# Performance work log

Hardware: AMD Instinct MI355X
Metric: run time of the kernel (lower is better)

## Reference

```python
import jax, jax.numpy as jnp
import numpy as np

BN_EPS = 1e-5

def _segment_mean(vals, idx, num_segments):
    s = jax.ops.segment_sum(vals, idx, num_segments=num_segments)
    cnt = jax.ops.segment_sum(jnp.ones((vals.shape[0],), vals.dtype), idx, num_segments=num_segments)
    return s / jnp.maximum(cnt, 1.0)[:, None]


def setup_inputs() -> dict:
    N, E, L = 50000, 800000, 1600000
    ND, ED = 256, 128
    key = jax.random.key(0)
    ks = jax.random.split(key, 8)
    return {
        "x": jax.random.normal(ks[0], (N, ND), jnp.float32),
        "edge_attr": jax.random.normal(ks[1], (E, ED), jnp.float32),
        "W_proj": jax.random.normal(ks[2], (ED, ND), jnp.float32) / np.sqrt(ND),
        "W1": jax.random.normal(ks[3], (ED, ED), jnp.float32) / np.sqrt(ED),
        "b1": jnp.zeros((ED,), jnp.float32),
        "prelu_a": jnp.full((1,), 0.25, jnp.float32),
        "bn_gamma": jnp.ones((ED,), jnp.float32),
        "bn_beta": jnp.zeros((ED,), jnp.float32),
        "edge_index": jax.random.randint(ks[4], (2, E), 0, N, jnp.int32),
        "line_graph_edge_index": jax.random.randint(ks[5], (2, L), 0, E, jnp.int32),
    }


def reference(x, edge_attr, W_proj, W1, b1, prelu_a, bn_gamma, bn_beta, edge_index, line_graph_edge_index):
    N = x.shape[0]
    E = edge_attr.shape[0]
    src, dst = edge_index[0], edge_index[1]
    # project once then gather (same math as gathering then projecting)
    px = x @ W_proj.T  # [N, edge_dim]
    fused = edge_attr + (px[src] + px[dst]) * 0.5  # [E, edge_dim]
    # line-graph message passing: scatter-mean over destination edges
    line_src, line_dst = line_graph_edge_index[0], line_graph_edge_index[1]
    agg = _segment_mean(fused[line_src], line_dst, E)  # [E, edge_dim]
    # edge update: Linear -> PReLU -> BatchNorm1d (training-mode batch stats)
    h = agg @ W1.T + b1
    h = jnp.where(h >= 0, h, prelu_a * h)
    mean = jnp.mean(h, axis=0)
    var = jnp.mean(jnp.square(h - mean), axis=0)  # biased, as torch BN
    h = (h - mean) * jax.lax.rsqrt(var + BN_EPS) * bn_gamma + bn_beta
    fused = fused + h
    # aggregate edges back to nodes (scatter-mean over dst)
    node_updates = _segment_mean(fused, dst, N)  # [N, edge_dim]
    return node_updates
```

## Files before the change

kernel.cpp:

```cpp
#include <hip/hip_runtime.h>
#include <cstdint>

#define BN_EPS 1e-5f

template<int K, bool EPI>
__global__ __launch_bounds__(256) void gemm_kernel(
    const float* __restrict__ A,
    const float* __restrict__ W,
    const float* __restrict__ bias,
    const float* __restrict__ prelu_a,
    float* __restrict__ C,
    float* __restrict__ bnsum,
    float* __restrict__ bnsumsq,
    int M)
{
    constexpr int BM = 64, BN = 128, BK = 32;
    __shared__ float aT[BK][BM + 4];
    __shared__ float wT[BK][BN];
    __shared__ float red_s[BN];
    __shared__ float red_q[BN];

    const int tid = threadIdx.x;
    const int tx = tid & 31;
    const int ty = tid >> 5;
    const int row0 = blockIdx.x * BM;

    float acc[8][4];
#pragma unroll
    for (int r = 0; r < 8; ++r)
#pragma unroll
        for (int c = 0; c < 4; ++c) acc[r][c] = 0.f;

    for (int k0 = 0; k0 < K; k0 += BK) {
#pragma unroll
        for (int rep = 0; rep < 2; ++rep) {
            int r  = (tid >> 3) + rep * 32;
            int kq = tid & 7;
            int grow = row0 + r;
            float4 v = make_float4(0.f, 0.f, 0.f, 0.f);
            if (grow < M)
                v = *(const float4*)(A + (size_t)grow * K + k0 + 4 * kq);
            aT[4*kq+0][r] = v.x;
            aT[4*kq+1][r] = v.y;
            aT[4*kq+2][r] = v.z;
            aT[4*kq+3][r] = v.w;
        }
#pragma unroll
        for (int rep = 0; rep < 4; ++rep) {
            int j  = tid & 127;
            int kh = tid >> 7;
            int kk = kh * 16 + rep * 4;
            float4 v = *(const float4*)(W + (size_t)j * K + k0 + kk);
            wT[kk+0][j] = v.x;
            wT[kk+1][j] = v.y;
            wT[kk+2][j] = v.z;
            wT[kk+3][j] = v.w;
        }
        __syncthreads();
#pragma unroll
        for (int k = 0; k < BK; ++k) {
            float4 w4 = *(const float4*)&wT[k][4*tx];
            float4 a0 = *(const float4*)&aT[k][8*ty];
            float4 a1 = *(const float4*)&aT[k][8*ty+4];
            float av[8] = {a0.x,a0.y,a0.z,a0.w,a1.x,a1.y,a1.z,a1.w};
            float wv[4] = {w4.x,w4.y,w4.z,w4.w};
#pragma unroll
            for (int r = 0; r < 8; ++r)
#pragma unroll
                for (int c = 0; c < 4; ++c)
                    acc[r][c] = fmaf(av[r], wv[c], acc[r][c]);
        }
        __syncthreads();
    }

    if (!EPI) {
#pragma unroll
        for (int r = 0; r < 8; ++r) {
            int grow = row0 + 8*ty + r;
            if (grow < M) {
                float4 o = make_float4(acc[r][0], acc[r][1], acc[r][2], acc[r][3]);
                *(float4*)(C + (size_t)grow * BN + 4*tx) = o;
            }
        }
    } else {
        float b[4];
#pragma unroll
        for (int c = 0; c < 4; ++c) b[c] = bias[4*tx + c];
        float pa = prelu_a[0];
        if (tid < BN) { red_s[tid] = 0.f; red_q[tid] = 0.f; }
        __syncthreads();
        float lsum[4] = {0,0,0,0}, lsq[4] = {0,0,0,0};
#pragma unroll
        for (int r = 0; r < 8; ++r) {
            int grow = row0 + 8*ty + r;
            if (grow < M) {
                float vv[4];
#pragma unroll
                for (int c = 0; c < 4; ++c) {
                    float v = acc[r][c] + b[c];
                    v = (v >= 0.f) ? v : pa * v;
                    vv[c] = v;
                    lsum[c] += v;
                    lsq[c]  += v * v;
                }
                float4 o = make_float4(vv[0], vv[1], vv[2], vv[3]);
                *(float4*)(C + (size_t)grow * BN + 4*tx) = o;
            }
        }
#pragma unroll
        for (int c = 0; c < 4; ++c) {
            atomicAdd(&red_s[4*tx + c], lsum[c]);
            atomicAdd(&red_q[4*tx + c], lsq[c]);
        }
        __syncthreads();
        if (tid < BN) {
            atomicAdd(&bnsum[tid],   red_s[tid]);
            atomicAdd(&bnsumsq[tid], red_q[tid]);
        }
    }
}

__global__ __launch_bounds__(256) void fuse_kernel(
    const float* __restrict__ edge_attr, const float* __restrict__ px,
    const int* __restrict__ src, const int* __restrict__ dst,
    float* __restrict__ fused, int E)
{
    size_t i = (size_t)blockIdx.x * blockDim.x + threadIdx.x;
    size_t total = (size_t)E * 32;
    if (i >= total) return;
    int e = (int)(i >> 5);
    int q = (int)(i & 31);
    int s = src[e], d = dst[e];
    float4 ea = ((const float4*)edge_attr)[i];
    float4 ps = ((const float4*)px)[(size_t)s * 32 + q];
    float4 pd = ((const float4*)px)[(size_t)d * 32 + q];
    float4 o;
    o.x = ea.x + 0.5f * (ps.x + pd.x);
    o.y = ea.y + 0.5f * (ps.y + pd.y);
    o.z = ea.z + 0.5f * (ps.z + pd.z);
    o.w = ea.w + 0.5f * (ps.w + pd.w);
    ((float4*)fused)[i] = o;
}

__global__ __launch_bounds__(256) void hist_kernel(
    const int* __restrict__ idx, int* __restrict__ deg, int n)
{
    int i = blockIdx.x * 256 + threadIdx.x;
    if (i < n) atomicAdd(&deg[idx[i]], 1);
}

__global__ __launch_bounds__(256) void scan_local_kernel(
    const int* __restrict__ deg, int* __restrict__ excl,
    int* __restrict__ bsum, int n)
{
    __shared__ int ts[256];
    int t = threadIdx.x;
    int base = blockIdx.x * 2048 + t * 8;
    int v[8]; int s = 0;
#pragma unroll
    for (int j = 0; j < 8; ++j) { v[j] = (base + j < n) ? deg[base + j] : 0; s += v[j]; }
    ts[t] = s; __syncthreads();
    for (int off = 1; off < 256; off <<= 1) {
        int x = (t >= off) ? ts[t - off] : 0;
        __syncthreads();
        ts[t] += x;
        __syncthreads();
    }
    if (t == 255) bsum[blockIdx.x] = ts[255];
    int run = ts[t] - s;
#pragma unroll
    for (int j = 0; j < 8; ++j) {
        if (base + j < n) excl[base + j] = run;
        run += v[j];
    }
}

__global__ __launch_bounds__(256) void scan_blocks_kernel(int* __restrict__ bsum, int nb)
{
    __shared__ int ts[256];
    __shared__ int carry_s;
    int t = threadIdx.x;
    if (t == 0) carry_s = 0;
    __syncthreads();
    for (int c0 = 0; c0 < nb; c0 += 256) {
        int v = (c0 + t < nb) ? bsum[c0 + t] : 0;
        ts[t] = v; __syncthreads();
        for (int off = 1; off < 256; off <<= 1) {
            int x = (t >= off) ? ts[t - off] : 0;
            __syncthreads();
            ts[t] += x;
            __syncthreads();
        }
        int carry = carry_s;
        if (c0 + t < nb) bsum[c0 + t] = carry + ts[t] - v;
        int tot = ts[255];
        __syncthreads();
        if (t == 0) carry_s = carry + tot;
        __syncthreads();
    }
}

__global__ __launch_bounds__(256) void scan_add_kernel(
    int* __restrict__ rowptr, const int* __restrict__ bsum,
    int* __restrict__ cursor, int n, int total)
{
    int i = blockIdx.x * 256 + threadIdx.x;
    if (i == 0) rowptr[n] = total;
    if (i >= n) return;
    int v = rowptr[i] + bsum[i >> 11];
    rowptr[i] = v;
    cursor[i] = v;
}

__global__ __launch_bounds__(256) void fill_kernel(
    const int* __restrict__ dsti, const int* __restrict__ vals,
    int* __restrict__ cursor, int* __restrict__ adj, int n)
{
    int i = blockIdx.x * 256 + threadIdx.x;
    if (i >= n) return;
    int pos = atomicAdd(&cursor[dsti[i]], 1);
    adj[pos] = vals ? vals[i] : i;
}

__global__ __launch_bounds__(256) void gather_line_kernel(
    const float* __restrict__ fused, const int* __restrict__ rowptr,
    const int* __restrict__ adj, float* __restrict__ agg, int E)
{
    int w = (int)(((size_t)blockIdx.x * 256 + threadIdx.x) >> 6);
    int lane = threadIdx.x & 63;
    if (w >= E) return;
    int s0 = rowptr[w], s1 = rowptr[w + 1];
    float2 acc = make_float2(0.f, 0.f);
    for (int j = s0; j < s1; ++j) {
        int s = adj[j];
        float2 v = ((const float2*)(fused + (size_t)s * 128))[lane];
        acc.x += v.x; acc.y += v.y;
    }
    float scl = 1.f / fmaxf((float)(s1 - s0), 1.f);
    ((float2*)(agg + (size_t)w * 128))[lane] = make_float2(acc.x * scl, acc.y * scl);
}

__global__ void bn_finalize_kernel(
    const float* __restrict__ bnsum, const float* __restrict__ bnsumsq,
    const float* __restrict__ gamma, const float* __restrict__ beta,
    float* __restrict__ cA, float* __restrict__ cB, float invE)
{
    int c = threadIdx.x;
    float mean = bnsum[c] * invE;
    float var  = bnsumsq[c] * invE - mean * mean;
    float istd = 1.f / sqrtf(var + BN_EPS);
    float a = istd * gamma[c];
    cA[c] = a;
    cB[c] = beta[c] - mean * a;
}

__global__ __launch_bounds__(256) void gather_node_kernel(
    const float* __restrict__ fused, const float* __restrict__ h,
    const int* __restrict__ rowptr, const int* __restrict__ adj,
    const float* __restrict__ cA, const float* __restrict__ cB,
    float* __restrict__ out, int N)
{
    int w = (int)(((size_t)blockIdx.x * 256 + threadIdx.x) >> 6);
    int lane = threadIdx.x & 63;
    if (w >= N) return;
    int s0 = rowptr[w], s1 = rowptr[w + 1];
    float2 A = ((const float2*)cA)[lane];
    float2 B = ((const float2*)cB)[lane];
    float2 acc = make_float2(0.f, 0.f);
    for (int j = s0; j < s1; ++j) {
        int e = adj[j];
        float2 f  = ((const float2*)(fused + (size_t)e * 128))[lane];
        float2 hh = ((const float2*)(h     + (size_t)e * 128))[lane];
        acc.x += f.x + fmaf(hh.x, A.x, B.x);
        acc.y += f.y + fmaf(hh.y, A.y, B.y);
    }
    float scl = 1.f / fmaxf((float)(s1 - s0), 1.f);
    ((float2*)(out + (size_t)w * 128))[lane] = make_float2(acc.x * scl, acc.y * scl);
}

extern "C" void kernel_launch(void* const* d_in, const int* in_sizes, int n_in,
                              void* d_out, int out_size, void* d_ws, size_t ws_size,
                              hipStream_t stream) {
    const float* x     = (const float*)d_in[0];
    const float* ea    = (const float*)d_in[1];
    const float* Wp    = (const float*)d_in[2];
    const float* W1    = (const float*)d_in[3];
    const float* b1    = (const float*)d_in[4];
    const float* pa    = (const float*)d_in[5];
    const float* gamma = (const float*)d_in[6];
    const float* beta  = (const float*)d_in[7];
    const int*   ei    = (const int*)d_in[8];
    const int*   lg    = (const int*)d_in[9];

    const int ND = 256, ED = 128;
    const int N = in_sizes[0] / ND;
    const int E = in_sizes[1] / ED;
    const int L = in_sizes[9] / 2;
    const int* src  = ei;
    const int* dstI = ei + E;
    const int* ls   = lg;
    const int* ld   = lg + L;

    float* ws = (float*)d_ws;
    size_t off = 0;
    float* px    = ws + off; off += (size_t)N * ED;
    float* fused = ws + off; off += (size_t)E * ED;
    float* aggh  = ws + off; off += (size_t)E * ED;
    float* bnsum = ws + off; off += ED;
    float* bnsq  = ws + off; off += ED;
    float* cA    = ws + off; off += ED;
    float* cB    = ws + off; off += ED;

    int* iws = (int*)(ws + off);
    size_t ioff = 0;
    int* deg_l  = iws + ioff; ioff += E;
    int* rp_l   = iws + ioff; ioff += E + 1;
    int* adj_l  = iws + ioff; ioff += L;
    int* bs_l   = iws + ioff; ioff += 1024;
    int* deg_n  = iws + ioff; ioff += N;
    int* rp_n   = iws + ioff; ioff += N + 1;
    int* adj_n  = iws + ioff; ioff += E;
    int* bs_n   = iws + ioff; ioff += 1024;

    float* out = (float*)d_out;

    const int nb_l = (E + 2047) / 2048;
    const int nb_n = (N + 2047) / 2048;

    hipMemsetAsync(bnsum, 0, 2 * ED * sizeof(float), stream);
    hipMemsetAsync(deg_l, 0, (size_t)E * sizeof(int), stream);
    hipMemsetAsync(deg_n, 0, (size_t)N * sizeof(int), stream);

    gemm_kernel<256, false><<<(N + 63) / 64, 256, 0, stream>>>(
        x, Wp, nullptr, nullptr, px, nullptr, nullptr, N);

    {
        size_t tot = (size_t)E * 32;
        fuse_kernel<<<(int)((tot + 255) / 256), 256, 0, stream>>>(ea, px, src, dstI, fused, E);
    }

    hist_kernel<<<(L + 255) / 256, 256, 0, stream>>>(ld, deg_l, L);
    scan_local_kernel<<<nb_l, 256, 0, stream>>>(deg_l, rp_l, bs_l, E);
    scan_blocks_kernel<<<1, 256, 0, stream>>>(bs_l, nb_l);
    scan_add_kernel<<<(E + 255) / 256, 256, 0, stream>>>(rp_l, bs_l, deg_l, E, L);
    fill_kernel<<<(L + 255) / 256, 256, 0, stream>>>(ld, ls, deg_l, adj_l, L);

    hist_kernel<<<(E + 255) / 256, 256, 0, stream>>>(dstI, deg_n, E);
    scan_local_kernel<<<nb_n, 256, 0, stream>>>(deg_n, rp_n, bs_n, N);
    scan_blocks_kernel<<<1, 256, 0, stream>>>(bs_n, nb_n);
    scan_add_kernel<<<(N + 255) / 256, 256, 0, stream>>>(rp_n, bs_n, deg_n, N, E);
    fill_kernel<<<(E + 255) / 256, 256, 0, stream>>>(dstI, nullptr, deg_n, adj_n, E);

    gather_line_kernel<<<(E + 3) / 4, 256, 0, stream>>>(fused, rp_l, adj_l, aggh, E);

    gemm_kernel<128, true><<<(E + 63) / 64, 256, 0, stream>>>(
        aggh, W1, b1, pa, aggh, bnsum, bnsq, E);

    bn_finalize_kernel<<<1, 128, 0, stream>>>(bnsum, bnsq, gamma, beta, cA, cB, 1.f / (float)E);

    gather_node_kernel<<<(N + 3) / 4, 256, 0, stream>>>(fused, aggh, rp_n, adj_n, cA, cB, out, N);
}
```

Baseline: 2.077 ms.

## Replace edge-update GEMM with persistent bf16x3 MFMA kernel using async LDS loads

Swaps the scalar-FMA fused Linear+PReLU+BN-stats GEMM for a persistent 512-thread kernel. It emulates fp32 with three bf16 MFMA passes (hi/lo split) and holds W in LDS as pre-split bf16. It double-buffers A tiles via global_load_lds and accumulates the BN statistics across all tiles before one atomic flush per block. The line-graph gather now writes agg in an XOR-swizzled layout to avoid LDS bank conflicts when the GEMM reads it. The bf16x3 split adds some rounding error versus true fp32, and the fixed 256-block grid may underuse or overload CUs.

```diff
diff --git a/kernel.cpp b/kernel.cpp
--- a/kernel.cpp
+++ b/kernel.cpp
@@ -2,6 +2,24 @@
 #include <cstdint>
 
 #define BN_EPS 1e-5f
+
+typedef __attribute__((ext_vector_type(8))) short bf16x8;
+typedef __attribute__((ext_vector_type(4))) float f32x4;
+
+#define GLD16(dst, src)                                                        \
+  __builtin_amdgcn_global_load_lds(                                            \
+      (const __attribute__((address_space(1))) void*)(src),                    \
+      (__attribute__((address_space(3))) void*)(dst), 16, 0, 0)
+
+__device__ inline void split8(const float* f, bf16x8& hi, bf16x8& lo) {
+#pragma unroll
+  for (int j = 0; j < 8; ++j) {
+    unsigned u = __float_as_uint(f[j]);
+    hi[j] = (short)(u >> 16);
+    float r = f[j] - __uint_as_float(u & 0xFFFF0000u);
+    lo[j] = (short)(__float_as_uint(r) >> 16);
+  }
+}
 
 template<int K, bool EPI>
 __global__ __launch_bounds__(256) void gemm_kernel(
@@ -17,8 +35,6 @@
     constexpr int BM = 64, BN = 128, BK = 32;
     __shared__ float aT[BK][BM + 4];
     __shared__ float wT[BK][BN];
-    __shared__ float red_s[BN];
-    __shared__ float red_q[BN];
 
     const int tid = threadIdx.x;
     const int tx = tid & 31;
@@ -73,50 +89,142 @@
         __syncthreads();
     }
 
-    if (!EPI) {
-#pragma unroll
-        for (int r = 0; r < 8; ++r) {
-            int grow = row0 + 8*ty + r;
-            if (grow < M) {
-                float4 o = make_float4(acc[r][0], acc[r][1], acc[r][2], acc[r][3]);
-                *(float4*)(C + (size_t)grow * BN + 4*tx) = o;
+#pragma unroll
+    for (int r = 0; r < 8; ++r) {
+        int grow = row0 + 8*ty + r;
+        if (grow < M) {
+            float4 o = make_float4(acc[r][0], acc[r][1], acc[r][2], acc[r][3]);
+            *(float4*)(C + (size_t)grow * BN + 4*tx) = o;
+        }
+    }
+    (void)bias; (void)prelu_a; (void)bnsum; (void)bnsumsq;
+}
+
+__global__ __launch_bounds__(512, 1) void gemm_h_kernel(
+    const float* __restrict__ A,
+    const float* __restrict__ W,
+    const float* __restrict__ bias,
+    const float* __restrict__ prelu_a,
+    float* __restrict__ C,
+    float* __restrict__ bnsum, float* __restrict__ bnsumsq, int M)
+{
+    __shared__ float  Abuf[2][64 * 128];
+    __shared__ bf16x8 Wh[32 * 64];
+    __shared__ bf16x8 Wl[32 * 64];
+    __shared__ float  red_s[128], red_q[128];
+
+    const int tid = threadIdx.x;
+    const int l   = tid & 63;
+    const int w   = tid >> 6;
+    const int rt  = w >> 1;
+    const int ch  = w & 1;
+    const int lr  = l & 15;
+    const int ks  = l >> 4;
+
+#pragma unroll
+    for (int pp = 0; pp < 4; ++pp) {
+        int p  = w * 4 + pp;
+        int kc = p >> 3, n = p & 7;
+        int col = n * 16 + lr;
+        int k0  = kc * 32 + ks * 8;
+        const float* wp = W + (size_t)col * 128 + k0;
+        float f[8];
+        *(float4*)&f[0] = *(const float4*)wp;
+        *(float4*)&f[4] = *(const float4*)(wp + 4);
+        bf16x8 hi, lo;
+        split8(f, hi, lo);
+        Wh[p * 64 + l] = hi;
+        Wl[p * 64 + l] = lo;
+    }
+
+    const int T = (M + 63) / 64;
+    const float pa = prelu_a[0];
+    float b_c[4];
+#pragma unroll
+    for (int nn = 0; nn < 4; ++nn) b_c[nn] = bias[ch * 64 + nn * 16 + lr];
+
+    float lsum[4] = {0.f,0.f,0.f,0.f}, lsq[4] = {0.f,0.f,0.f,0.f};
+
+    const int t0 = blockIdx.x;
+    const int G  = gridDim.x;
+
+    auto stage = [&](int buf, int t) {
+#pragma unroll
+        for (int p = 0; p < 4; ++p) {
+            int chunk = p * 512 + tid;
+            int row   = chunk >> 5;
+            long grow = (long)t * 64 + row;
+            if (grow >= M) grow = M - 1;
+            const char* src = (const char*)A + grow * 512 + (size_t)(chunk & 31) * 16;
+            char* dst = (char*)&Abuf[buf][0] + (size_t)chunk * 16;
+            GLD16(dst, src);
+        }
+    };
+
+    if (t0 < T) stage(0, t0);
+    __syncthreads();
+
+    for (int i = 0, t = t0; t < T; ++i, t += G) {
+        int cur = i & 1;
+        int tn = t + G;
+        if (tn < T) stage(cur ^ 1, tn);
+
+        f32x4 acc[4];
+#pragma unroll
+        for (int nn = 0; nn < 4; ++nn) acc[nn] = (f32x4){0.f,0.f,0.f,0.f};
+
+        const float* Ab = &Abuf[cur][0];
+        const int r = rt * 16 + lr;
+#pragma unroll
+        for (int kc = 0; kc < 4; ++kc) {
+            int seg = (kc * 4 + ks) ^ lr;
+            const float* ap = Ab + r * 128 + seg * 8;
+            float f[8];
+            *(float4*)&f[0] = *(const float4*)ap;
+            *(float4*)&f[4] = *(const float4*)(ap + 4);
+            bf16x8 ah, al;
+            split8(f, ah, al);
+#pragma unroll
+            for (int nn = 0; nn < 4; ++nn) {
+                int p = kc * 8 + (ch * 4 + nn);
+                bf16x8 bh = Wh[p * 64 + l];
+                bf16x8 bl = Wl[p * 64 + l];
+                acc[nn] = __builtin_amdgcn_mfma_f32_16x16x32_bf16(ah, bh, acc[nn], 0, 0, 0);
+                acc[nn] = __builtin_amdgcn_mfma_f32_16x16x32_bf16(ah, bl, acc[nn], 0, 0, 0);
+                acc[nn] = __builtin_amdgcn_mfma_f32_16x16x32_bf16(al, bh, acc[nn], 0, 0, 0);
             }
         }
-    } else {
-        float b[4];
-#pragma unroll
-        for (int c = 0; c < 4; ++c) b[c] = bias[4*tx + c];
-        float pa = prelu_a[0];
-        if (tid < BN) { red_s[tid] = 0.f; red_q[tid] = 0.f; }
-        __syncthreads();
-        float lsum[4] = {0,0,0,0}, lsq[4] = {0,0,0,0};
-#pragma unroll
-        for (int r = 0; r < 8; ++r) {
-            int grow = row0 + 8*ty + r;
-            if (grow < M) {
-                float vv[4];
-#pragma unroll
-                for (int c = 0; c < 4; ++c) {
-                    float v = acc[r][c] + b[c];
+
+#pragma unroll
+        for (int nn = 0; nn < 4; ++nn) {
+            int col = ch * 64 + nn * 16 + lr;
+#pragma unroll
+            for (int reg = 0; reg < 4; ++reg) {
+                long grow = (long)t * 64 + rt * 16 + ks * 4 + reg;
+                if (grow < M) {
+                    float v = acc[nn][reg] + b_c[nn];
                     v = (v >= 0.f) ? v : pa * v;
-                    vv[c] = v;
-                    lsum[c] += v;
-                    lsq[c]  += v * v;
+                    C[grow * 128 + col] = v;
+                    lsum[nn] += v;
+                    lsq[nn]  += v * v;
                 }
-                float4 o = make_float4(vv[0], vv[1], vv[2], vv[3]);
-                *(float4*)(C + (size_t)grow * BN + 4*tx) = o;
             }
         }
-#pragma unroll
-        for (int c = 0; c < 4; ++c) {
-            atomicAdd(&red_s[4*tx + c], lsum[c]);
-            atomicAdd(&red_q[4*tx + c], lsq[c]);
-        }
-        __syncthreads();
-        if (tid < BN) {
-            atomicAdd(&bnsum[tid],   red_s[tid]);
-            atomicAdd(&bnsumsq[tid], red_q[tid]);
-        }
+        __syncthreads();
+    }
+
+    if (tid < 128) { red_s[tid] = 0.f; red_q[tid] = 0.f; }
+    __syncthreads();
+#pragma unroll
+    for (int nn = 0; nn < 4; ++nn) {
+        int col = ch * 64 + nn * 16 + lr;
+        atomicAdd(&red_s[col], lsum[nn]);
+        atomicAdd(&red_q[col], lsq[nn]);
+    }
+    __syncthreads();
+    if (tid < 128) {
+        atomicAdd(&bnsum[tid],   red_s[tid]);
+        atomicAdd(&bnsumsq[tid], red_q[tid]);
     }
 }
 
@@ -237,7 +345,10 @@
         acc.x += v.x; acc.y += v.y;
     }
     float scl = 1.f / fmaxf((float)(s1 - s0), 1.f);
-    ((float2*)(agg + (size_t)w * 128))[lane] = make_float2(acc.x * scl, acc.y * scl);
+    int seg = lane >> 2;
+    int sw  = seg ^ (w & 15);
+    *(float2*)((char*)agg + (size_t)w * 512 + ((size_t)sw << 5) + ((size_t)(lane & 3) << 3))
+        = make_float2(acc.x * scl, acc.y * scl);
 }
 
 __global__ void bn_finalize_kernel(
@@ -353,8 +464,7 @@
 
     gather_line_kernel<<<(E + 3) / 4, 256, 0, stream>>>(fused, rp_l, adj_l, aggh, E);
 
-    gemm_kernel<128, true><<<(E + 63) / 64, 256, 0, stream>>>(
-        aggh, W1, b1, pa, aggh, bnsum, bnsq, E);
+    gemm_h_kernel<<<256, 512, 0, stream>>>(aggh, W1, b1, pa, aggh, bnsum, bnsq, E);
 
     bn_finalize_kernel<<<1, 128, 0, stream>>>(bnsum, bnsq, gamma, beta, cA, cB, 1.f / (float)E);
 
```

New measurement: 1.804 ms. 13.2% less time.
